# Performance work log

Hardware: AMD Instinct MI355X
Metric: run time of the kernel (lower is better)

## Reference

```python
import jax, jax.numpy as jnp
import numpy as np

MARGIN = 1.0
N, D = 8192, 128
NUM_CLASSES = 43


def setup_inputs() -> dict:
    key = jax.random.key(0)
    kx, ky = jax.random.split(key)
    x = jax.random.normal(kx, (N, D), dtype=jnp.float32)
    y = jax.random.randint(ky, (N,), 0, NUM_CLASSES, dtype=jnp.int64)
    return {"x": x, "y": y}


def reference(x, y):
    # Pairwise squared distances between rows of x: [N, N].
    # Equivalent to the original tile/permute construction, but via GEMM:
    # ||a-b||^2 = ||a||^2 + ||b||^2 - 2 a.b
    sq = jnp.sum(x * x, axis=1)                      # [N]
    norms = sq[:, None] + sq[None, :] - 2.0 * (x @ x.T)  # [N, N]
    maxims = jnp.maximum(MARGIN - norms, 0.0)        # [N, N]

    # Same-label mask (1 where labels equal, 0 otherwise).
    equalities = (y[:, None] == y[None, :]).astype(norms.dtype)  # [N, N]
    eye = jnp.eye(x.shape[0], dtype=norms.dtype)

    pos_mask = equalities - eye       # positive pairs, excluding self
    neg_mask = 1.0 - equalities       # negative pairs

    pos_term = jnp.sum(pos_mask * norms) / jnp.sum(pos_mask)
    neg_term = jnp.sum(neg_mask * maxims) / jnp.sum(neg_mask)
    return (pos_term + neg_term) / 2.0
```

## Files before the change

### kernel.cpp

```cpp
#include <hip/hip_runtime.h>

#define N_ROWS 8192
#define DIM 128
#define NCLS 43
#define TILE 128
#define TILES 64
#define NPAIRS 2080

typedef __attribute__((ext_vector_type(4))) float float4v;
typedef __attribute__((address_space(1))) const void global_cvoid;
typedef __attribute__((address_space(3))) void lds_void;

#define SM_B   16384
#define SM_SQA 32768
#define SM_SQB 33280
#define SM_YA  33792
#define SM_YB  34304
#define SM_RED 34816
#define SM_SIZE 34880

__global__ void __launch_bounds__(256) prep_kernel(
        const float* __restrict__ x,
        float* __restrict__ sq,
        unsigned char* __restrict__ xq) {
    int wave = threadIdx.x >> 6;
    int lane = threadIdx.x & 63;
    int half = lane >> 5, l32 = lane & 31;
    int row  = blockIdx.x * 8 + wave * 2 + half;
    const float4 v = *(const float4*)(x + (size_t)row * DIM + l32 * 4);
    int pk = __builtin_amdgcn_cvt_pk_fp8_f32(v.x, v.y, 0, 0);
    pk     = __builtin_amdgcn_cvt_pk_fp8_f32(v.z, v.w, pk, 1);
    *(int*)(xq + (size_t)row * DIM + l32 * 4) = pk;
    float s = v.x * v.x + v.y * v.y + v.z * v.z + v.w * v.w;
    #pragma unroll
    for (int off = 16; off > 0; off >>= 1) s += __shfl_down(s, off);
    if (l32 == 0) sq[row] = s;
}

__global__ void __launch_bounds__(256, 4) tile_kernel(
        const unsigned char* __restrict__ xq,
        const float* __restrict__ sq,
        const int* __restrict__ y,
        float2* __restrict__ partials) {
    __shared__ __align__(16) char smem[SM_SIZE];

    int t = blockIdx.x;
    int bi = (int)((129.0f - sqrtf((float)(129 * 129 - 8 * t))) * 0.5f);
    if (bi < 0) bi = 0;
    if (bi > TILES - 1) bi = TILES - 1;
    while (bi * TILES - (bi * (bi - 1)) / 2 > t) --bi;
    while ((bi + 1) * TILES - ((bi + 1) * bi) / 2 <= t) ++bi;
    int bj = bi + (t - (bi * TILES - (bi * (bi - 1)) / 2));

    int wv   = threadIdx.x >> 6;
    int lane = threadIdx.x & 63;

    const char* srcA = (const char*)(xq + (size_t)bi * TILE * DIM);
    const char* srcB = (const char*)(xq + (size_t)bj * TILE * DIM);
    #pragma unroll
    for (int it = 0; it < 4; ++it) {
        int pbase = (it * 4 + wv) * 1024;
        int p = pbase + lane * 16;
        int r = p >> 7;
        int c = ((p >> 4) & 7) ^ (r & 7);
        int goff = (r << 7) + (c << 4);
        __builtin_amdgcn_global_load_lds(
            (global_cvoid*)(srcA + goff), (lds_void*)(smem + pbase), 16, 0, 0);
        __builtin_amdgcn_global_load_lds(
            (global_cvoid*)(srcB + goff), (lds_void*)(smem + SM_B + pbase), 16, 0, 0);
    }
    {
        int ti = threadIdx.x;
        if (ti < 128)  ((float*)(smem + SM_SQA))[ti]       = sq[bi * TILE + ti];
        else           ((float*)(smem + SM_SQB))[ti - 128] = sq[bj * TILE + ti - 128];
        if (ti < 128)  ((int*)  (smem + SM_YA ))[ti]       = y [bi * TILE + ti];
        else           ((int*)  (smem + SM_YB ))[ti - 128] = y [bj * TILE + ti - 128];
    }
    __syncthreads();

    int m    = lane & 15;
    int quad = lane >> 4;
    int wr   = (wv >> 1) * 64;
    int wc   = (wv & 1) * 64;

    float4v acc[4][4];
    #pragma unroll
    for (int a = 0; a < 4; ++a)
        #pragma unroll
        for (int c = 0; c < 4; ++c) {
            float4v z = {0.f, 0.f, 0.f, 0.f};
            acc[a][c] = z;
        }

    int halfoff = (quad & 1) * 8;
    #pragma unroll
    for (int ks = 0; ks < 4; ++ks) {
        int cl = ks * 2 + (quad >> 1);
        long af[4], bfr[4];
        #pragma unroll
        for (int ti = 0; ti < 4; ++ti) {
            int R = wr + ti * 16 + m;
            af[ti] = *(const long*)(smem + R * 128 + ((cl ^ (R & 7)) << 4) + halfoff);
        }
        #pragma unroll
        for (int tj = 0; tj < 4; ++tj) {
            int R = wc + tj * 16 + m;
            bfr[tj] = *(const long*)(smem + SM_B + R * 128 + ((cl ^ (R & 7)) << 4) + halfoff);
        }
        #pragma unroll
        for (int ti = 0; ti < 4; ++ti)
            #pragma unroll
            for (int tj = 0; tj < 4; ++tj)
                acc[ti][tj] = __builtin_amdgcn_mfma_f32_16x16x32_fp8_fp8(
                                  af[ti], bfr[tj], acc[ti][tj], 0, 0, 0);
    }

    const float* sqA = (const float*)(smem + SM_SQA);
    const float* sqB = (const float*)(smem + SM_SQB);
    const int*   yA  = (const int*)  (smem + SM_YA);
    const int*   yB  = (const int*)  (smem + SM_YB);
    int ibase = wr + quad * 4;
    int jbase = wc + m;

    float sqj[4]; int yj[4];
    #pragma unroll
    for (int tj = 0; tj < 4; ++tj) {
        sqj[tj] = sqB[jbase + tj * 16];
        yj[tj]  = yB [jbase + tj * 16];
    }
    float sqjmin = fminf(fminf(sqj[0], sqj[1]), fminf(sqj[2], sqj[3]));
    float posD = 0.f, dotmax = -3e38f, sqimin = 3e38f;

    if (bi != bj) {
        #pragma unroll
        for (int ti = 0; ti < 4; ++ti) {
            #pragma unroll
            for (int r = 0; r < 4; ++r) {
                int il = ibase + ti * 16 + r;
                float sqi = sqA[il]; int yi = yA[il];
                sqimin = fminf(sqimin, sqi);
                #pragma unroll
                for (int tj = 0; tj < 4; ++tj) {
                    float d = acc[ti][tj][r];
                    posD += (yi == yj[tj]) ? d : 0.f;
                    dotmax = fmaxf(dotmax, d);
                }
            }
        }
    } else {
        #pragma unroll
        for (int ti = 0; ti < 4; ++ti) {
            #pragma unroll
            for (int r = 0; r < 4; ++r) {
                int il = ibase + ti * 16 + r;
                float sqi = sqA[il]; int yi = yA[il];
                sqimin = fminf(sqimin, sqi);
                #pragma unroll
                for (int tj = 0; tj < 4; ++tj) {
                    int jl = jbase + tj * 16;
                    bool self = (il == jl);
                    float d = acc[ti][tj][r];
                    posD += (yi == yj[tj] && !self) ? d : 0.f;
                    dotmax = fmaxf(dotmax, self ? -3e38f : d);
                }
            }
        }
    }

    float negS = 0.f;
    if (2.f * dotmax - sqimin - sqjmin >= -1.f) {
        #pragma unroll
        for (int ti = 0; ti < 4; ++ti)
            #pragma unroll
            for (int r = 0; r < 4; ++r) {
                int il = ibase + ti * 16 + r;
                float sqi = sqA[il]; int yi = yA[il];
                #pragma unroll
                for (int tj = 0; tj < 4; ++tj)
                    if (yi != yj[tj]) {
                        float nrm = fmaf(-2.f, acc[ti][tj][r], sqi + sqj[tj]);
                        negS += fmaxf(1.f - nrm, 0.f);
                    }
            }
    }
    float wgt = (bi == bj) ? 1.f : 2.f;
    float posP = wgt * posD;
    float negP = wgt * negS;

    #pragma unroll
    for (int off = 32; off > 0; off >>= 1) {
        posP += __shfl_down(posP, off);
        negP += __shfl_down(negP, off);
    }
    float2* wred = (float2*)(smem + SM_RED);
    if (lane == 0) wred[wv] = make_float2(posP, negP);
    __syncthreads();
    if (threadIdx.x == 0) {
        float2 a0 = wred[0], a1 = wred[1], a2 = wred[2], a3 = wred[3];
        partials[t] = make_float2(a0.x + a1.x + a2.x + a3.x,
                                  a0.y + a1.y + a2.y + a3.y);
    }
}

__global__ void __launch_bounds__(1024) finish_kernel(
        const float2* __restrict__ partials,
        const int* __restrict__ y,
        const float* __restrict__ sq,
        float* __restrict__ out) {
    __shared__ int hists[16][48];
    __shared__ int htot[48];
    __shared__ float2 red[16];
    __shared__ float swred[16];
    int tid = threadIdx.x, wv = tid >> 6, lane = tid & 63;

    for (int i = tid; i < 16 * 48; i += 1024) ((int*)hists)[i] = 0;
    __syncthreads();

    const int4* y4 = (const int4*)y;
    int4 ya = y4[tid], yb = y4[tid + 1024];
    atomicAdd(&hists[wv][ya.x], 1); atomicAdd(&hists[wv][ya.y], 1);
    atomicAdd(&hists[wv][ya.z], 1); atomicAdd(&hists[wv][ya.w], 1);
    atomicAdd(&hists[wv][yb.x], 1); atomicAdd(&hists[wv][yb.y], 1);
    atomicAdd(&hists[wv][yb.z], 1); atomicAdd(&hists[wv][yb.w], 1);
    __syncthreads();
    if (tid < 48) {
        int nc = 0;
        #pragma unroll
        for (int w = 0; w < 16; ++w) nc += hists[w][tid];
        htot[tid] = nc;
    }
    __syncthreads();

    const float4* sq4 = (const float4*)sq;
    float4 sa = sq4[tid], sb = sq4[tid + 1024];
    float sw = sa.x * (float)(htot[ya.x] - 1) + sa.y * (float)(htot[ya.y] - 1)
             + sa.z * (float)(htot[ya.z] - 1) + sa.w * (float)(htot[ya.w] - 1)
             + sb.x * (float)(htot[yb.x] - 1) + sb.y * (float)(htot[yb.y] - 1)
             + sb.z * (float)(htot[yb.z] - 1) + sb.w * (float)(htot[yb.w] - 1);

    float p = 0.f, n = 0.f;
    for (int i = tid; i < NPAIRS; i += 1024) {
        float2 v = partials[i];
        p += v.x; n += v.y;
    }
    #pragma unroll
    for (int off = 32; off > 0; off >>= 1) {
        sw += __shfl_down(sw, off);
        p  += __shfl_down(p, off);
        n  += __shfl_down(n, off);
    }
    if (lane == 0) { red[wv] = make_float2(p, n); swred[wv] = sw; }
    __syncthreads();
    if (tid == 0) {
        float PS = 0.f, NS = 0.f, SW = 0.f;
        #pragma unroll
        for (int w = 0; w < 16; ++w) { PS += red[w].x; NS += red[w].y; SW += swred[w]; }
        long long s2 = 0;
        for (int c = 0; c < NCLS; ++c) { long long h = htot[c]; s2 += h * h; }
        float posc = (float)(s2 - (long long)N_ROWS);
        float negc = (float)((long long)N_ROWS * N_ROWS - s2);
        out[0] = 0.5f * ((2.f * SW - 2.f * PS) / posc + NS / negc);
    }
}

extern "C" void kernel_launch(void* const* d_in, const int* in_sizes, int n_in,
                              void* d_out, int out_size, void* d_ws, size_t ws_size,
                              hipStream_t stream) {
    const float* x = (const float*)d_in[0];
    const int*   y = (const int*)d_in[1];
    float* out = (float*)d_out;

    char* ws = (char*)d_ws;
    float2*         partials = (float2*)ws;
    float*          sq       = (float*)(ws + 16896);
    unsigned char*  xq       = (unsigned char*)(ws + 49920);

    prep_kernel<<<N_ROWS / 8, 256, 0, stream>>>(x, sq, xq);
    tile_kernel<<<NPAIRS, 256, 0, stream>>>(xq, sq, y, partials);
    finish_kernel<<<1, 1024, 0, stream>>>(partials, y, sq, out);
}
```

Before: 74.50 us.

## Compute positive term via class sums and add block-level early exit for negatives

Replaces the per-pair positive-distance accumulation with a closed form built from per-class feature sums (sum of ||c_k||^2) computed in the prep kernel and reduced by extra blocks in the tile kernel. The negative-term skip test now uses per-64-row precomputed minimum squared norms, and the squared norms and labels are read from global memory instead of staged in LDS. Per-tile partials are replaced by a global atomicAdd only when a tile passes the test. The aim is to cut epilogue arithmetic and LDS staging in the tile kernel. In exchange the prep kernel does many LDS float atomics, and fp32 atomic accumulation makes the result order-dependent. The skip threshold moves from -1 to -33, which looks like slack for the coarser bound or fp8 error.

```diff
diff --git a/kernel.cpp b/kernel.cpp
--- a/kernel.cpp
+++ b/kernel.cpp
@@ -6,45 +6,102 @@
 #define TILE 128
 #define TILES 64
 #define NPAIRS 2080
+#define NRED 64
+#define PREPB 128
+#define CS_ENT (NCLS * DIM)
+#define ENT_PER_RED 86
 
 typedef __attribute__((ext_vector_type(4))) float float4v;
 typedef __attribute__((address_space(1))) const void global_cvoid;
 typedef __attribute__((address_space(3))) void lds_void;
 
 #define SM_B   16384
-#define SM_SQA 32768
-#define SM_SQB 33280
-#define SM_YA  33792
-#define SM_YB  34304
-#define SM_RED 34816
-#define SM_SIZE 34880
-
-__global__ void __launch_bounds__(256) prep_kernel(
-        const float* __restrict__ x,
-        float* __restrict__ sq,
-        unsigned char* __restrict__ xq) {
-    int wave = threadIdx.x >> 6;
-    int lane = threadIdx.x & 63;
-    int half = lane >> 5, l32 = lane & 31;
-    int row  = blockIdx.x * 8 + wave * 2 + half;
-    const float4 v = *(const float4*)(x + (size_t)row * DIM + l32 * 4);
-    int pk = __builtin_amdgcn_cvt_pk_fp8_f32(v.x, v.y, 0, 0);
-    pk     = __builtin_amdgcn_cvt_pk_fp8_f32(v.z, v.w, pk, 1);
-    *(int*)(xq + (size_t)row * DIM + l32 * 4) = pk;
-    float s = v.x * v.x + v.y * v.y + v.z * v.z + v.w * v.w;
-    #pragma unroll
-    for (int off = 16; off > 0; off >>= 1) s += __shfl_down(s, off);
-    if (l32 == 0) sq[row] = s;
+#define SM_SIZE 32768
+
+__global__ void __launch_bounds__(512) prep_kernel(
+        const float* __restrict__ x, const int* __restrict__ y,
+        float* __restrict__ sq, float* __restrict__ sqmin,
+        float* __restrict__ cspart, unsigned char* __restrict__ xq,
+        float* __restrict__ negacc) {
+    __shared__ float cs[CS_ENT];
+    __shared__ float rsq[64];
+    int tid = threadIdx.x;
+    for (int i = tid; i < CS_ENT; i += 512) cs[i] = 0.f;
+    if (blockIdx.x == 0 && tid == 0) *negacc = 0.f;
+    __syncthreads();
+
+    int rloc = tid >> 3;
+    int seg  = tid & 7;
+    int row  = blockIdx.x * 64 + rloc;
+    const float4* px = (const float4*)(x + (size_t)row * DIM + seg * 16);
+    float4 v0 = px[0], v1 = px[1], v2 = px[2], v3 = px[3];
+
+    int q0 = __builtin_amdgcn_cvt_pk_fp8_f32(v0.x, v0.y, 0, 0);
+    q0     = __builtin_amdgcn_cvt_pk_fp8_f32(v0.z, v0.w, q0, 1);
+    int q1 = __builtin_amdgcn_cvt_pk_fp8_f32(v1.x, v1.y, 0, 0);
+    q1     = __builtin_amdgcn_cvt_pk_fp8_f32(v1.z, v1.w, q1, 1);
+    int q2 = __builtin_amdgcn_cvt_pk_fp8_f32(v2.x, v2.y, 0, 0);
+    q2     = __builtin_amdgcn_cvt_pk_fp8_f32(v2.z, v2.w, q2, 1);
+    int q3 = __builtin_amdgcn_cvt_pk_fp8_f32(v3.x, v3.y, 0, 0);
+    q3     = __builtin_amdgcn_cvt_pk_fp8_f32(v3.z, v3.w, q3, 1);
+    *(int4*)(xq + (size_t)row * DIM + seg * 16) = make_int4(q0, q1, q2, q3);
+
+    float s = v0.x*v0.x + v0.y*v0.y + v0.z*v0.z + v0.w*v0.w
+            + v1.x*v1.x + v1.y*v1.y + v1.z*v1.z + v1.w*v1.w
+            + v2.x*v2.x + v2.y*v2.y + v2.z*v2.z + v2.w*v2.w
+            + v3.x*v3.x + v3.y*v3.y + v3.z*v3.z + v3.w*v3.w;
+    s += __shfl_xor(s, 1); s += __shfl_xor(s, 2); s += __shfl_xor(s, 4);
+    if (seg == 0) { sq[row] = s; rsq[rloc] = s; }
+
+    int yr = y[row];
+    float* c = &cs[yr * DIM + seg * 16];
+    atomicAdd(&c[0],  v0.x); atomicAdd(&c[1],  v0.y); atomicAdd(&c[2],  v0.z); atomicAdd(&c[3],  v0.w);
+    atomicAdd(&c[4],  v1.x); atomicAdd(&c[5],  v1.y); atomicAdd(&c[6],  v1.z); atomicAdd(&c[7],  v1.w);
+    atomicAdd(&c[8],  v2.x); atomicAdd(&c[9],  v2.y); atomicAdd(&c[10], v2.z); atomicAdd(&c[11], v2.w);
+    atomicAdd(&c[12], v3.x); atomicAdd(&c[13], v3.y); atomicAdd(&c[14], v3.z); atomicAdd(&c[15], v3.w);
+    __syncthreads();
+
+    for (int i = tid; i < CS_ENT; i += 512)
+        cspart[(size_t)blockIdx.x * CS_ENT + i] = cs[i];
+    if (tid < 64) {
+        float mn = rsq[tid];
+        #pragma unroll
+        for (int off = 32; off > 0; off >>= 1) mn = fminf(mn, __shfl_down(mn, off));
+        if (tid == 0) sqmin[blockIdx.x] = mn;
+    }
 }
 
 __global__ void __launch_bounds__(256, 4) tile_kernel(
         const unsigned char* __restrict__ xq,
         const float* __restrict__ sq,
         const int* __restrict__ y,
-        float2* __restrict__ partials) {
+        const float* __restrict__ sqmin,
+        const float* __restrict__ cspart,
+        float* __restrict__ csred,
+        float* __restrict__ negacc) {
     __shared__ __align__(16) char smem[SM_SIZE];
-
-    int t = blockIdx.x;
+    int tid = threadIdx.x;
+
+    if (blockIdx.x < NRED) {
+        int rb = blockIdx.x;
+        float ssum = 0.f;
+        if (tid < ENT_PER_RED) {
+            int e = rb * ENT_PER_RED + tid;
+            float S = 0.f;
+            for (int b = 0; b < PREPB; ++b) S += cspart[(size_t)b * CS_ENT + e];
+            ssum = S * S;
+        }
+        #pragma unroll
+        for (int off = 32; off > 0; off >>= 1) ssum += __shfl_down(ssum, off);
+        float* red = (float*)smem;
+        int wv = tid >> 6, lane = tid & 63;
+        if (lane == 0) red[wv] = ssum;
+        __syncthreads();
+        if (tid == 0) csred[rb] = red[0] + red[1] + red[2] + red[3];
+        return;
+    }
+
+    int t = blockIdx.x - NRED;
     int bi = (int)((129.0f - sqrtf((float)(129 * 129 - 8 * t))) * 0.5f);
     if (bi < 0) bi = 0;
     if (bi > TILES - 1) bi = TILES - 1;
@@ -52,8 +109,8 @@
     while ((bi + 1) * TILES - ((bi + 1) * bi) / 2 <= t) ++bi;
     int bj = bi + (t - (bi * TILES - (bi * (bi - 1)) / 2));
 
-    int wv   = threadIdx.x >> 6;
-    int lane = threadIdx.x & 63;
+    int wv   = tid >> 6;
+    int lane = tid & 63;
 
     const char* srcA = (const char*)(xq + (size_t)bi * TILE * DIM);
     const char* srcB = (const char*)(xq + (size_t)bj * TILE * DIM);
@@ -69,13 +126,6 @@
         __builtin_amdgcn_global_load_lds(
             (global_cvoid*)(srcB + goff), (lds_void*)(smem + SM_B + pbase), 16, 0, 0);
     }
-    {
-        int ti = threadIdx.x;
-        if (ti < 128)  ((float*)(smem + SM_SQA))[ti]       = sq[bi * TILE + ti];
-        else           ((float*)(smem + SM_SQB))[ti - 128] = sq[bj * TILE + ti - 128];
-        if (ti < 128)  ((int*)  (smem + SM_YA ))[ti]       = y [bi * TILE + ti];
-        else           ((int*)  (smem + SM_YB ))[ti - 128] = y [bj * TILE + ti - 128];
-    }
     __syncthreads();
 
     int m    = lane & 15;
@@ -115,101 +165,62 @@
                                   af[ti], bfr[tj], acc[ti][tj], 0, 0, 0);
     }
 
-    const float* sqA = (const float*)(smem + SM_SQA);
-    const float* sqB = (const float*)(smem + SM_SQB);
-    const int*   yA  = (const int*)  (smem + SM_YA);
-    const int*   yB  = (const int*)  (smem + SM_YB);
     int ibase = wr + quad * 4;
     int jbase = wc + m;
-
-    float sqj[4]; int yj[4];
-    #pragma unroll
-    for (int tj = 0; tj < 4; ++tj) {
-        sqj[tj] = sqB[jbase + tj * 16];
-        yj[tj]  = yB [jbase + tj * 16];
-    }
-    float sqjmin = fminf(fminf(sqj[0], sqj[1]), fminf(sqj[2], sqj[3]));
-    float posD = 0.f, dotmax = -3e38f, sqimin = 3e38f;
-
+    float dm = -3e38f;
     if (bi != bj) {
         #pragma unroll
-        for (int ti = 0; ti < 4; ++ti) {
+        for (int ti = 0; ti < 4; ++ti)
+            #pragma unroll
+            for (int tj = 0; tj < 4; ++tj) {
+                float4v a4 = acc[ti][tj];
+                dm = fmaxf(dm, fmaxf(fmaxf(a4[0], a4[1]), fmaxf(a4[2], a4[3])));
+            }
+    } else {
+        #pragma unroll
+        for (int ti = 0; ti < 4; ++ti)
             #pragma unroll
             for (int r = 0; r < 4; ++r) {
                 int il = ibase + ti * 16 + r;
-                float sqi = sqA[il]; int yi = yA[il];
-                sqimin = fminf(sqimin, sqi);
                 #pragma unroll
                 for (int tj = 0; tj < 4; ++tj) {
-                    float d = acc[ti][tj][r];
-                    posD += (yi == yj[tj]) ? d : 0.f;
-                    dotmax = fmaxf(dotmax, d);
+                    bool self = (il == jbase + tj * 16);
+                    dm = fmaxf(dm, self ? -3e38f : acc[ti][tj][r]);
                 }
             }
-        }
-    } else {
-        #pragma unroll
-        for (int ti = 0; ti < 4; ++ti) {
+    }
+
+    float smi = fminf(sqmin[2 * bi], sqmin[2 * bi + 1]);
+    float smj = fminf(sqmin[2 * bj], sqmin[2 * bj + 1]);
+    if (2.f * dm - smi - smj >= -33.f) {
+        float negS = 0.f;
+        #pragma unroll
+        for (int ti = 0; ti < 4; ++ti)
             #pragma unroll
             for (int r = 0; r < 4; ++r) {
-                int il = ibase + ti * 16 + r;
-                float sqi = sqA[il]; int yi = yA[il];
-                sqimin = fminf(sqimin, sqi);
+                int gi = bi * TILE + ibase + ti * 16 + r;
+                float sqi = sq[gi]; int yi = y[gi];
                 #pragma unroll
                 for (int tj = 0; tj < 4; ++tj) {
-                    int jl = jbase + tj * 16;
-                    bool self = (il == jl);
-                    float d = acc[ti][tj][r];
-                    posD += (yi == yj[tj] && !self) ? d : 0.f;
-                    dotmax = fmaxf(dotmax, self ? -3e38f : d);
+                    int gj = bj * TILE + jbase + tj * 16;
+                    if (gi != gj && yi != y[gj]) {
+                        float nrm = fmaf(-2.f, acc[ti][tj][r], sqi + sq[gj]);
+                        negS += fmaxf(1.f - nrm, 0.f);
+                    }
                 }
             }
-        }
-    }
-
-    float negS = 0.f;
-    if (2.f * dotmax - sqimin - sqjmin >= -1.f) {
-        #pragma unroll
-        for (int ti = 0; ti < 4; ++ti)
-            #pragma unroll
-            for (int r = 0; r < 4; ++r) {
-                int il = ibase + ti * 16 + r;
-                float sqi = sqA[il]; int yi = yA[il];
-                #pragma unroll
-                for (int tj = 0; tj < 4; ++tj)
-                    if (yi != yj[tj]) {
-                        float nrm = fmaf(-2.f, acc[ti][tj][r], sqi + sqj[tj]);
-                        negS += fmaxf(1.f - nrm, 0.f);
-                    }
-            }
-    }
-    float wgt = (bi == bj) ? 1.f : 2.f;
-    float posP = wgt * posD;
-    float negP = wgt * negS;
-
-    #pragma unroll
-    for (int off = 32; off > 0; off >>= 1) {
-        posP += __shfl_down(posP, off);
-        negP += __shfl_down(negP, off);
-    }
-    float2* wred = (float2*)(smem + SM_RED);
-    if (lane == 0) wred[wv] = make_float2(posP, negP);
-    __syncthreads();
-    if (threadIdx.x == 0) {
-        float2 a0 = wred[0], a1 = wred[1], a2 = wred[2], a3 = wred[3];
-        partials[t] = make_float2(a0.x + a1.x + a2.x + a3.x,
-                                  a0.y + a1.y + a2.y + a3.y);
+        atomicAdd(negacc, ((bi == bj) ? 1.f : 2.f) * negS);
     }
 }
 
 __global__ void __launch_bounds__(1024) finish_kernel(
-        const float2* __restrict__ partials,
         const int* __restrict__ y,
         const float* __restrict__ sq,
+        const float* __restrict__ csred,
+        const float* __restrict__ negacc,
         float* __restrict__ out) {
     __shared__ int hists[16][48];
     __shared__ int htot[48];
-    __shared__ float2 red[16];
     __shared__ float swred[16];
     int tid = threadIdx.x, wv = tid >> 6, lane = tid & 63;
 
@@ -233,33 +244,25 @@
 
     const float4* sq4 = (const float4*)sq;
     float4 sa = sq4[tid], sb = sq4[tid + 1024];
-    float sw = sa.x * (float)(htot[ya.x] - 1) + sa.y * (float)(htot[ya.y] - 1)
-             + sa.z * (float)(htot[ya.z] - 1) + sa.w * (float)(htot[ya.w] - 1)
-             + sb.x * (float)(htot[yb.x] - 1) + sb.y * (float)(htot[yb.y] - 1)
-             + sb.z * (float)(htot[yb.z] - 1) + sb.w * (float)(htot[yb.w] - 1);
-
-    float p = 0.f, n = 0.f;
-    for (int i = tid; i < NPAIRS; i += 1024) {
-        float2 v = partials[i];
-        p += v.x; n += v.y;
-    }
-    #pragma unroll
-    for (int off = 32; off > 0; off >>= 1) {
-        sw += __shfl_down(sw, off);
-        p  += __shfl_down(p, off);
-        n  += __shfl_down(n, off);
-    }
-    if (lane == 0) { red[wv] = make_float2(p, n); swred[wv] = sw; }
+    float sw = sa.x * (float)htot[ya.x] + sa.y * (float)htot[ya.y]
+             + sa.z * (float)htot[ya.z] + sa.w * (float)htot[ya.w]
+             + sb.x * (float)htot[yb.x] + sb.y * (float)htot[yb.y]
+             + sb.z * (float)htot[yb.z] + sb.w * (float)htot[yb.w];
+    #pragma unroll
+    for (int off = 32; off > 0; off >>= 1) sw += __shfl_down(sw, off);
+    if (lane == 0) swred[wv] = sw;
     __syncthreads();
     if (tid == 0) {
-        float PS = 0.f, NS = 0.f, SW = 0.f;
-        #pragma unroll
-        for (int w = 0; w < 16; ++w) { PS += red[w].x; NS += red[w].y; SW += swred[w]; }
+        float SW = 0.f;
+        #pragma unroll
+        for (int w = 0; w < 16; ++w) SW += swred[w];
+        float CS = 0.f;
+        for (int r = 0; r < NRED; ++r) CS += csred[r];
         long long s2 = 0;
         for (int c = 0; c < NCLS; ++c) { long long h = htot[c]; s2 += h * h; }
         float posc = (float)(s2 - (long long)N_ROWS);
         float negc = (float)((long long)N_ROWS * N_ROWS - s2);
-        out[0] = 0.5f * ((2.f * SW - 2.f * PS) / posc + NS / negc);
+        out[0] = 0.5f * (2.f * (SW - CS) / posc + negacc[0] / negc);
     }
 }
 
@@ -271,11 +274,14 @@
     float* out = (float*)d_out;
 
     char* ws = (char*)d_ws;
-    float2*         partials = (float2*)ws;
-    float*          sq       = (float*)(ws + 16896);
-    unsigned char*  xq       = (unsigned char*)(ws + 49920);
-
-    prep_kernel<<<N_ROWS / 8, 256, 0, stream>>>(x, sq, xq);
-    tile_kernel<<<NPAIRS, 256, 0, stream>>>(xq, sq, y, partials);
-    finish_kernel<<<1, 1024, 0, stream>>>(partials, y, sq, out);
-}
+    float*          negacc = (float*)ws;
+    float*          sqmin  = (float*)(ws + 256);
+    float*          sq     = (float*)(ws + 1024);
+    float*          csred  = (float*)(ws + 33792);
+    float*          cspart = (float*)(ws + 34304);
+    unsigned char*  xq     = (unsigned char*)(ws + 3145728);
+
+    prep_kernel<<<PREPB, 512, 0, stream>>>(x, y, sq, sqmin, cspart, xq, negacc);
+    tile_kernel<<<NRED + NPAIRS, 256, 0, stream>>>(xq, sq, y, sqmin, cspart, csred, negacc);
+    finish_kernel<<<1, 1024, 0, stream>>>(y, sq, csred, negacc, out);
+}
```

Measured after the change: 82.90 us. 1.11x slower.

## Use 16x16x128 scaled FP8 MFMA and read sq/labels directly from global

Applied to the files above, without the earlier changes.

Replaces the four-step K loop of 16x16x32 FP8 MFMAs with a single 16x16x128 scaled MFMA per output tile, loading 32-byte fragments from swizzled LDS. This cuts the MFMA instruction count and LDS read count. It also stops staging sq and labels in LDS and reads them from global/cache in the epilogue, which shrinks LDS use. The LDS reduction buffer is reused, which needs an extra barrier, and a self-pair guard is added to the negative term.

```diff
diff --git a/kernel.cpp b/kernel.cpp
--- a/kernel.cpp
+++ b/kernel.cpp
@@ -8,16 +8,13 @@
 #define NPAIRS 2080
 
 typedef __attribute__((ext_vector_type(4))) float float4v;
+typedef __attribute__((ext_vector_type(4))) int   int4v;
+typedef __attribute__((ext_vector_type(8))) int   int8v;
 typedef __attribute__((address_space(1))) const void global_cvoid;
 typedef __attribute__((address_space(3))) void lds_void;
 
-#define SM_B   16384
-#define SM_SQA 32768
-#define SM_SQB 33280
-#define SM_YA  33792
-#define SM_YB  34304
-#define SM_RED 34816
-#define SM_SIZE 34880
+#define SM_B    16384
+#define SM_SIZE 32768
 
 __global__ void __launch_bounds__(256) prep_kernel(
         const float* __restrict__ x,
@@ -69,13 +66,6 @@
         __builtin_amdgcn_global_load_lds(
             (global_cvoid*)(srcB + goff), (lds_void*)(smem + SM_B + pbase), 16, 0, 0);
     }
-    {
-        int ti = threadIdx.x;
-        if (ti < 128)  ((float*)(smem + SM_SQA))[ti]       = sq[bi * TILE + ti];
-        else           ((float*)(smem + SM_SQB))[ti - 128] = sq[bj * TILE + ti - 128];
-        if (ti < 128)  ((int*)  (smem + SM_YA ))[ti]       = y [bi * TILE + ti];
-        else           ((int*)  (smem + SM_YB ))[ti - 128] = y [bj * TILE + ti - 128];
-    }
     __syncthreads();
 
     int m    = lane & 15;
@@ -92,41 +82,42 @@
             acc[a][c] = z;
         }
 
-    int halfoff = (quad & 1) * 8;
-    #pragma unroll
-    for (int ks = 0; ks < 4; ++ks) {
-        int cl = ks * 2 + (quad >> 1);
-        long af[4], bfr[4];
-        #pragma unroll
-        for (int ti = 0; ti < 4; ++ti) {
-            int R = wr + ti * 16 + m;
-            af[ti] = *(const long*)(smem + R * 128 + ((cl ^ (R & 7)) << 4) + halfoff);
-        }
-        #pragma unroll
-        for (int tj = 0; tj < 4; ++tj) {
-            int R = wc + tj * 16 + m;
-            bfr[tj] = *(const long*)(smem + SM_B + R * 128 + ((cl ^ (R & 7)) << 4) + halfoff);
-        }
+    int8v af[4];
+    #pragma unroll
+    for (int ti = 0; ti < 4; ++ti) {
+        int R = wr + ti * 16 + m;
+        const char* base = smem + R * 128;
+        int4v lo = *(const int4v*)(base + ((( 2 * quad     ) ^ (R & 7)) << 4));
+        int4v hi = *(const int4v*)(base + (((2 * quad + 1) ^ (R & 7)) << 4));
+        int8v v; v[0]=lo[0]; v[1]=lo[1]; v[2]=lo[2]; v[3]=lo[3];
+                 v[4]=hi[0]; v[5]=hi[1]; v[6]=hi[2]; v[7]=hi[3];
+        af[ti] = v;
+    }
+    #pragma unroll
+    for (int tj = 0; tj < 4; ++tj) {
+        int R = wc + tj * 16 + m;
+        const char* base = smem + SM_B + R * 128;
+        int4v lo = *(const int4v*)(base + ((( 2 * quad     ) ^ (R & 7)) << 4));
+        int4v hi = *(const int4v*)(base + (((2 * quad + 1) ^ (R & 7)) << 4));
+        int8v bv; bv[0]=lo[0]; bv[1]=lo[1]; bv[2]=lo[2]; bv[3]=lo[3];
+                  bv[4]=hi[0]; bv[5]=hi[1]; bv[6]=hi[2]; bv[7]=hi[3];
         #pragma unroll
         for (int ti = 0; ti < 4; ++ti)
-            #pragma unroll
-            for (int tj = 0; tj < 4; ++tj)
-                acc[ti][tj] = __builtin_amdgcn_mfma_f32_16x16x32_fp8_fp8(
-                                  af[ti], bfr[tj], acc[ti][tj], 0, 0, 0);
-    }
-
-    const float* sqA = (const float*)(smem + SM_SQA);
-    const float* sqB = (const float*)(smem + SM_SQB);
-    const int*   yA  = (const int*)  (smem + SM_YA);
-    const int*   yB  = (const int*)  (smem + SM_YB);
-    int ibase = wr + quad * 4;
-    int jbase = wc + m;
+            acc[ti][tj] = __builtin_amdgcn_mfma_scale_f32_16x16x128_f8f6f4(
+                af[ti], bv, acc[ti][tj],
+                0, 0,
+                0, 0x7F7F7F7F,
+                0, 0x7F7F7F7F);
+    }
+
+    int giB = bi * TILE + wr + quad * 4;
+    int gjB = bj * TILE + wc + m;
 
     float sqj[4]; int yj[4];
     #pragma unroll
     for (int tj = 0; tj < 4; ++tj) {
-        sqj[tj] = sqB[jbase + tj * 16];
-        yj[tj]  = yB [jbase + tj * 16];
+        sqj[tj] = sq[gjB + tj * 16];
+        yj[tj]  = y [gjB + tj * 16];
     }
     float sqjmin = fminf(fminf(sqj[0], sqj[1]), fminf(sqj[2], sqj[3]));
     float posD = 0.f, dotmax = -3e38f, sqimin = 3e38f;
@@ -136,8 +127,8 @@
         for (int ti = 0; ti < 4; ++ti) {
             #pragma unroll
             for (int r = 0; r < 4; ++r) {
-                int il = ibase + ti * 16 + r;
-                float sqi = sqA[il]; int yi = yA[il];
+                int gi = giB + ti * 16 + r;
+                float sqi = sq[gi]; int yi = y[gi];
                 sqimin = fminf(sqimin, sqi);
                 #pragma unroll
                 for (int tj = 0; tj < 4; ++tj) {
@@ -152,13 +143,12 @@
         for (int ti = 0; ti < 4; ++ti) {
             #pragma unroll
             for (int r = 0; r < 4; ++r) {
-                int il = ibase + ti * 16 + r;
-                float sqi = sqA[il]; int yi = yA[il];
+                int gi = giB + ti * 16 + r;
+                float sqi = sq[gi]; int yi = y[gi];
                 sqimin = fminf(sqimin, sqi);
                 #pragma unroll
                 for (int tj = 0; tj < 4; ++tj) {
-                    int jl = jbase + tj * 16;
-                    bool self = (il == jl);
+                    bool self = (gi == gjB + tj * 16);
                     float d = acc[ti][tj][r];
                     posD += (yi == yj[tj] && !self) ? d : 0.f;
                     dotmax = fmaxf(dotmax, self ? -3e38f : d);
@@ -173,14 +163,16 @@
         for (int ti = 0; ti < 4; ++ti)
             #pragma unroll
             for (int r = 0; r < 4; ++r) {
-                int il = ibase + ti * 16 + r;
-                float sqi = sqA[il]; int yi = yA[il];
+                int gi = giB + ti * 16 + r;
+                float sqi = sq[gi]; int yi = y[gi];
                 #pragma unroll
-                for (int tj = 0; tj < 4; ++tj)
-                    if (yi != yj[tj]) {
+                for (int tj = 0; tj < 4; ++tj) {
+                    int gj = gjB + tj * 16;
+                    if (gi != gj && yi != yj[tj]) {
                         float nrm = fmaf(-2.f, acc[ti][tj][r], sqi + sqj[tj]);
                         negS += fmaxf(1.f - nrm, 0.f);
                     }
+                }
             }
     }
     float wgt = (bi == bj) ? 1.f : 2.f;
@@ -192,7 +184,8 @@
         posP += __shfl_down(posP, off);
         negP += __shfl_down(negP, off);
     }
-    float2* wred = (float2*)(smem + SM_RED);
+    __syncthreads();
+    float2* wred = (float2*)smem;
     if (lane == 0) wred[wv] = make_float2(posP, negP);
     __syncthreads();
     if (threadIdx.x == 0) {
```

New measurement: 72.80 us. 1.02x faster.
